# Kernel optimization log

Hardware: AMD Instinct MI355X
Metric: run time of the kernel (lower is better)

Reference implementation:

```python
import jax, jax.numpy as jnp
import numpy as np

DIM = 512
HEADS = 16
HIDDEN = 2048
EPS = 1e-5


def _layernorm(x, g, b):
    mu = jnp.mean(x, axis=-1, keepdims=True)
    var = jnp.mean((x - mu) ** 2, axis=-1, keepdims=True)
    return (x - mu) * jax.lax.rsqrt(var + EPS) * g + b


def _heads_merge(o):
    # Faithful to source: sum.reshape(B, N, D) applied to [B, H, N, pd]
    # WITHOUT transposing heads back (reproduces the original bug).
    B, H, N, pd = o.shape
    return o.reshape(B, N, H * pd)


def _self_attn(x, w, b, H):
    B, N, D = x.shape
    pd = D // H
    qkv = (x @ w + b).reshape(B, N, 3, H, pd).transpose(2, 0, 3, 1, 4)
    q, k, v = qkv[0], qkv[1], qkv[2]
    # NOTE: no 1/sqrt(pd) scaling in the source.
    s = jax.nn.softmax(jnp.einsum('bhnd,bhmd->bhnm', q, k), axis=-1)
    o = jnp.einsum('bhnm,bhmd->bhnd', s, v)  # == broadcast-multiply-and-sum in source
    return _heads_merge(o)


def _cross_attn(x1, x2, qw, qb, kvw, kvb, H):
    B, N, D = x1.shape
    pd = D // H
    q = (x2 @ qw + qb).reshape(B, N, H, pd).transpose(0, 2, 1, 3)
    kv = (x1 @ kvw + kvb).reshape(B, N, 2, H, pd).transpose(2, 0, 3, 1, 4)
    k, v = kv[0], kv[1]
    s = jax.nn.softmax(jnp.einsum('bhnd,bhmd->bhnm', q, k), axis=-1)
    o = jnp.einsum('bhnm,bhmd->bhnd', s, v)
    return _heads_merge(o)


def setup_inputs() -> dict:
    key = jax.random.key(0)
    ks = jax.random.split(key, 16)
    B, N, D, Hd = 4, 2048, DIM, HIDDEN
    s = 0.02
    return {
        'x1': jax.random.normal(ks[0], (B, N, D), jnp.float32),
        'x2': jax.random.normal(ks[1], (B, N, D), jnp.float32),
        'qkv_w': jax.random.normal(ks[2], (D, 3 * D), jnp.float32) * s,
        'qkv_b': jnp.zeros((3 * D,), jnp.float32),
        'q_w': jax.random.normal(ks[3], (D, D), jnp.float32) * s,
        'q_b': jnp.zeros((D,), jnp.float32),
        'kv_w': jax.random.normal(ks[4], (D, 2 * D), jnp.float32) * s,
        'kv_b': jnp.zeros((2 * D,), jnp.float32),
        'norm_g': jnp.ones((D,), jnp.float32),
        'norm_b': jnp.zeros((D,), jnp.float32),
        'fc1_w': jax.random.normal(ks[5], (D, Hd), jnp.float32) * s,
        'fc1_b': jnp.zeros((Hd,), jnp.float32),
        'fc2_w': jax.random.normal(ks[6], (Hd, D), jnp.float32) * s,
        'fc2_b': jnp.zeros((D,), jnp.float32),
    }


def reference(x1, x2, qkv_w, qkv_b, q_w, q_b, kv_w, kv_b, norm_g, norm_b,
              fc1_w, fc1_b, fc2_w, fc2_b):
    # CrossSelfDecoder.forward
    x = x2 + _cross_attn(x1, x2, q_w, q_b, kv_w, kv_b, HEADS)
    n = _layernorm(x, norm_g, norm_b)  # same norm params reused (as in source)
    x = n + _self_attn(n, qkv_w, qkv_b, HEADS)
    n = _layernorm(x, norm_g, norm_b)
    h = jax.nn.gelu(n @ fc1_w + fc1_b, approximate=False)
    x = n + (h @ fc2_w + fc2_b)
    return x
```

## Files before the change

### kernel.cpp

```cpp
#include <hip/hip_runtime.h>
#include <math.h>

#define DIM 512
#define HEADS 16
#define PD 32
#define NSEQ 2048
#define BATCH 4
#define HIDDEN 2048
#define LOG2E 1.44269504088896f

typedef __attribute__((ext_vector_type(8))) __bf16 bf16x8;
typedef __attribute__((ext_vector_type(4))) float f32x4;
typedef __attribute__((ext_vector_type(16))) float f32x16;

__device__ __forceinline__ ushort f2bf(float f) {
    unsigned u = __float_as_uint(f);
    u = (u + 0x7FFFu + ((u >> 16) & 1u)) >> 16;
    return (ushort)u;
}

__device__ __forceinline__ unsigned cvtpk_bf16(float lo, float hi) {
    unsigned r;
    asm("v_cvt_pk_bf16_f32 %0, %1, %2" : "=v"(r) : "v"(lo), "v"(hi));
    return r;
}

__device__ __forceinline__ float exp2_fast(float x) {
    float r;
    asm("v_exp_f32 %0, %1" : "=v"(r) : "v"(x));
    return r;
}

typedef __attribute__((address_space(1))) const unsigned int g_u32;
typedef __attribute__((address_space(3))) unsigned int l_u32;
__device__ __forceinline__ void gload16(const void* g, void* l) {
    __builtin_amdgcn_global_load_lds((g_u32*)g, (l_u32*)l, 16, 0, 0);
}

__device__ __forceinline__ float gelu_exact(float v) {
    return 0.5f * v * (1.0f + erff(v * 0.70710678118654752f));
}

__global__ __launch_bounds__(256)
void tr_all_kernel(const float* __restrict__ q_w, const float* __restrict__ kv_w,
                   const float* __restrict__ qkv_w, const float* __restrict__ fc1_w,
                   const float* __restrict__ fc2_w, ushort* __restrict__ wtb)
{
    __shared__ float t[32][33];
    const int bid = blockIdx.x;
    const float* W; ushort* Wt; int K, N, lb;
    if (bid < 256)       { W = q_w;   Wt = wtb;           K = 512;  N = 512;  lb = bid; }
    else if (bid < 768)  { W = kv_w;  Wt = wtb + 262144;  K = 512;  N = 1024; lb = bid - 256; }
    else if (bid < 1536) { W = qkv_w; Wt = wtb + 786432;  K = 512;  N = 1536; lb = bid - 768; }
    else if (bid < 2560) { W = fc1_w; Wt = wtb + 1572864; K = 512;  N = 2048; lb = bid - 1536; }
    else                 { W = fc2_w; Wt = wtb + 2621440; K = 2048; N = 512;  lb = bid - 2560; }
    const int nx = N / 32;
    const int n0 = (lb % nx) * 32, k0 = (lb / nx) * 32;
    const int tid = threadIdx.x;
    const int c = tid & 31, r0 = tid >> 5;
    #pragma unroll
    for (int i = 0; i < 4; ++i) {
        int r = r0 + i * 8;
        t[r][c] = W[(size_t)(k0 + r) * N + n0 + c];
    }
    __syncthreads();
    #pragma unroll
    for (int i = 0; i < 4; ++i) {
        int r = r0 + i * 8;
        Wt[(size_t)(n0 + r) * K + k0 + c] = f2bf(t[c][r]);
    }
}

template<int AIN, int EPI>
__global__ __launch_bounds__(256)
void mgemm(const void* __restrict__ Ap, const ushort* __restrict__ Bt,
           const float* __restrict__ bias, const float* __restrict__ resp,
           void* __restrict__ Cp, ushort* __restrict__ vtp,
           int M, int K, int Nc, int qcols, int vcol0)
{
    __shared__ __align__(16) ushort As[128 * 32];
    __shared__ __align__(16) ushort Bs[128 * 32];

    const int tid = threadIdx.x;
    const int wid = tid >> 6, ln = tid & 63;
    const int g = ln >> 4, c = ln & 15;
    const int wr = wid >> 1, wc = wid & 1;

    const int nwg = gridDim.x * gridDim.y;
    const int lid = blockIdx.y * gridDim.x + blockIdx.x;
    const int wg  = (lid & 7) * (nwg >> 3) + (lid >> 3);
    const int by = wg / gridDim.x, bx = wg % gridDim.x;
    const int row0 = by * 128, col0 = bx * 128;

    const f32x4 fzero = {0.f, 0.f, 0.f, 0.f};
    f32x4 acc[4][4];
    #pragma unroll
    for (int i = 0; i < 4; ++i)
        #pragma unroll
        for (int j = 0; j < 4; ++j) acc[i][j] = fzero;

    const int srow = tid >> 1, skh = tid & 1;
    const int w3 = (srow >> 1) & 3;
    const int ws0 = (2 * skh) ^ w3, ws1 = (2 * skh + 1) ^ w3;
    ushort* asw0 = &As[srow * 32 + ws0 * 8];
    ushort* asw1 = &As[srow * 32 + ws1 * 8];
    ushort* bsw0 = &Bs[srow * 32 + ws0 * 8];
    ushort* bsw1 = &Bs[srow * 32 + ws1 * 8];

    const int ps = (c >> 1) & 3;

    for (int k0 = 0; k0 < K; k0 += 32) {
        if (AIN == 0) {
            const float4* ap = (const float4*)((const float*)Ap
                                + (size_t)(row0 + srow) * K + k0 + skh * 16);
            float4 f0 = ap[0], f1 = ap[1], f2 = ap[2], f3 = ap[3];
            union { ushort u[16]; uint4 v[2]; } t;
            t.u[0] = f2bf(f0.x);  t.u[1] = f2bf(f0.y);  t.u[2] = f2bf(f0.z);  t.u[3] = f2bf(f0.w);
            t.u[4] = f2bf(f1.x);  t.u[5] = f2bf(f1.y);  t.u[6] = f2bf(f1.z);  t.u[7] = f2bf(f1.w);
            t.u[8] = f2bf(f2.x);  t.u[9] = f2bf(f2.y);  t.u[10] = f2bf(f2.z); t.u[11] = f2bf(f2.w);
            t.u[12] = f2bf(f3.x); t.u[13] = f2bf(f3.y); t.u[14] = f2bf(f3.z); t.u[15] = f2bf(f3.w);
            *(uint4*)asw0 = t.v[0];
            *(uint4*)asw1 = t.v[1];
        } else {
            const uint4* ap = (const uint4*)((const ushort*)Ap
                                + (size_t)(row0 + srow) * K + k0 + skh * 16);
            *(uint4*)asw0 = ap[0];
            *(uint4*)asw1 = ap[1];
        }
        {
            const uint4* bp = (const uint4*)(Bt + (size_t)(col0 + srow) * K + k0 + skh * 16);
            *(uint4*)bsw0 = bp[0];
            *(uint4*)bsw1 = bp[1];
        }
        __syncthreads();

        bf16x8 a[4], b[4];
        #pragma unroll
        for (int mt = 0; mt < 4; ++mt)
            a[mt] = *(const bf16x8*)&As[(wr * 64 + mt * 16 + c) * 32 + ((g ^ ps) * 8)];
        #pragma unroll
        for (int nt = 0; nt < 4; ++nt)
            b[nt] = *(const bf16x8*)&Bs[(wc * 64 + nt * 16 + c) * 32 + ((g ^ ps) * 8)];

        #pragma unroll
        for (int mt = 0; mt < 4; ++mt)
            #pragma unroll
            for (int nt = 0; nt < 4; ++nt)
                acc[mt][nt] = __builtin_amdgcn_mfma_f32_16x16x32_bf16(a[mt], b[nt], acc[mt][nt], 0, 0, 0);
        __syncthreads();
    }

    float bs[4];
    #pragma unroll
    for (int nt = 0; nt < 4; ++nt) bs[nt] = bias[col0 + wc * 64 + nt * 16 + c];

    #pragma unroll
    for (int mt = 0; mt < 4; ++mt) {
        const int rb = row0 + wr * 64 + mt * 16 + g * 4;
        #pragma unroll
        for (int nt = 0; nt < 4; ++nt) {
            const int col = col0 + wc * 64 + nt * 16 + c;
            if (EPI == 3 && col >= vcol0) {
                int cc = col - vcol0;
                int hh = cc >> 5, pd = cc & 31;
                int bq = rb >> 11, ntok = rb & 2047;
                union { ushort u[4]; uint2 v; } pk;
                #pragma unroll
                for (int reg = 0; reg < 4; ++reg)
                    pk.u[reg] = f2bf(acc[mt][nt][reg] + bs[nt]);
                *(uint2*)&vtp[((size_t)(bq * 16 + hh) * 32 + pd) * 2048 + ntok] = pk.v;
            } else {
                #pragma unroll
                for (int reg = 0; reg < 4; ++reg) {
                    int r = rb + reg;
                    float v = acc[mt][nt][reg] + bs[nt];
                    if (EPI == 1) {
                        ((ushort*)Cp)[(size_t)r * Nc + col] = f2bf(gelu_exact(v));
                    } else if (EPI == 2) {
                        ((float*)Cp)[(size_t)r * Nc + col] = v + resp[(size_t)r * Nc + col];
                    } else {
                        float v2 = (col < qcols) ? v * LOG2E : v;
                        ((ushort*)Cp)[(size_t)r * Nc + col] = f2bf(v2);
                    }
                }
            }
        }
    }
}

__global__ __launch_bounds__(256)
void attn_mfma_kernel(const ushort* __restrict__ qb_, int qstride, int qoff,
                      const ushort* __restrict__ kb_, int kstride, int koff,
                      const ushort* __restrict__ vtg,
                      const float* res, const float* __restrict__ gptr,
                      const float* __restrict__ bptr,
                      float* nf32, ushort* __restrict__ nb16)
{
    __shared__ __align__(16) ushort Klds[2][128 * 32];
    __shared__ __align__(16) ushort Vtlds[2][32 * 128];

    const int tid = threadIdx.x;
    const int w   = tid >> 6;
    const int ln  = tid & 63;
    const int c32 = ln & 31;
    const int hi  = ln >> 5;

    const int bid = blockIdx.x;
    const int xcd = bid & 7, jj = bid >> 3;
    const int bh = xcd + 8 * (jj >> 4);
    const int qt = jj & 15;
    const int b = bh >> 4, h = bh & 15;
    const size_t rowbase = (size_t)b * NSEQ;
    const int qt0 = qt * 128 + w * 32;
    const int n = qt0 + c32;

    bf16x8 qfrag[2];
    #pragma unroll
    for (int ph = 0; ph < 2; ++ph)
        qfrag[ph] = *(const bf16x8*)(qb_ + (rowbase + n) * qstride + qoff
                                     + h * PD + ph * 16 + hi * 8);

    const ushort* ks[2];
    const ushort* vs[2];
    int kd[2], vd[2];
    #pragma unroll
    for (int i = 0; i < 2; ++i) {
        int ch = 2 * w + i;
        int kvc = ch * 16 + (ln >> 2);
        int q4  = (ln & 3) ^ ((kvc >> 1) & 3);
        ks[i] = kb_ + (rowbase + kvc) * kstride + koff + h * PD + q4 * 8;
        kd[i] = ch * 512;
        int pdc = ch * 4 + (ln >> 4);
        int kv0 = ((ln & 15) ^ (pdc & 15)) * 8;
        vs[i] = vtg + ((size_t)bh * PD + pdc) * 2048 + kv0;
        vd[i] = ch * 512;
    }

#define STAGE(bi, trow)                                              \
    {                                                                \
        gload16(ks[0] + (size_t)(trow) * kstride, &Klds[bi][kd[0]]); \
        gload16(ks[1] + (size_t)(trow) * kstride, &Klds[bi][kd[1]]); \
        gload16(vs[0] + (trow), &Vtlds[bi][vd[0]]);                  \
        gload16(vs[1] + (trow), &Vtlds[bi][vd[1]]);                  \
    }

    f32x16 oacc, zero16;
    #pragma unroll
    for (int i = 0; i < 16; ++i) { oacc[i] = 0.f; zero16[i] = 0.f; }
    float l = 0.f;

    STAGE(0, 0);

    for (int t = 0; t < NSEQ / 128; ++t) {
        __syncthreads();
        if (t < NSEQ / 128 - 1) STAGE((t + 1) & 1, (t + 1) * 128);
        const ushort* Kb = Klds[t & 1];
        const ushort* Vb = Vtlds[t & 1];

        #pragma unroll
        for (int hh = 0; hh < 2; ++hh) {
            bf16x8 kf[2][2];
            #pragma unroll
            for (int kt = 0; kt < 2; ++kt)
                #pragma unroll
                for (int ph = 0; ph < 2; ++ph) {
                    int slot = (2 * ph + hi) ^ ((c32 >> 1) & 3);
                    kf[kt][ph] = *(const bf16x8*)&Kb[(hh * 64 + kt * 32 + c32) * 32 + slot * 8];
                }
            bf16x8 vf[4];
            #pragma unroll
            for (int j = 0; j < 4; ++j) {
                int slot = (hh * 8 + 2 * j + hi) ^ (c32 & 15);
                vf[j] = *(const bf16x8*)&Vb[c32 * 128 + slot * 8];
            }

            f32x16 st[2];
            __builtin_amdgcn_s_setprio(1);
            #pragma unroll
            for (int kt = 0; kt < 2; ++kt) {
                st[kt] = __builtin_amdgcn_mfma_f32_32x32x16_bf16(kf[kt][0], qfrag[0], zero16, 0, 0, 0);
                st[kt] = __builtin_amdgcn_mfma_f32_32x32x16_bf16(kf[kt][1], qfrag[1], st[kt], 0, 0, 0);
            }
            __builtin_amdgcn_s_setprio(0);

            float r0 = 0.f, r1 = 0.f, r2 = 0.f, r3 = 0.f;
            #pragma unroll
            for (int kt = 0; kt < 2; ++kt) {
                #pragma unroll
                for (int i = 0; i < 4; ++i) {
                    float p0 = exp2_fast(st[kt][i * 4 + 0]);
                    float p1 = exp2_fast(st[kt][i * 4 + 1]);
                    float p2 = exp2_fast(st[kt][i * 4 + 2]);
                    float p3 = exp2_fast(st[kt][i * 4 + 3]);
                    st[kt][i * 4 + 0] = p0; r0 += p0;
                    st[kt][i * 4 + 1] = p1; r1 += p1;
                    st[kt][i * 4 + 2] = p2; r2 += p2;
                    st[kt][i * 4 + 3] = p3; r3 += p3;
                }
            }
            float rsum = (r0 + r1) + (r2 + r3);
            rsum += __shfl_xor(rsum, 32);
            l += rsum;

            unsigned wpk[2][4][2];
            #pragma unroll
            for (int kt = 0; kt < 2; ++kt)
                #pragma unroll
                for (int rg = 0; rg < 4; ++rg) {
                    wpk[kt][rg][0] = cvtpk_bf16(st[kt][rg * 4 + 0], st[kt][rg * 4 + 1]);
                    wpk[kt][rg][1] = cvtpk_bf16(st[kt][rg * 4 + 2], st[kt][rg * 4 + 3]);
                }

            __builtin_amdgcn_s_setprio(1);
            #pragma unroll
            for (int j = 0; j < 4; ++j) {
                int kt = j >> 1, rg0 = 2 * (j & 1);
                unsigned x0 = wpk[kt][rg0][0], y0 = wpk[kt][rg0 + 1][0];
                unsigned x1 = wpk[kt][rg0][1], y1 = wpk[kt][rg0 + 1][1];
                asm("v_permlane32_swap_b32 %0, %1" : "+v"(x0), "+v"(y0));
                asm("v_permlane32_swap_b32 %0, %1" : "+v"(x1), "+v"(y1));
                union { unsigned u[4]; bf16x8 v; } pf;
                pf.u[0] = x0; pf.u[1] = x1; pf.u[2] = y0; pf.u[3] = y1;
                oacc = __builtin_amdgcn_mfma_f32_32x32x16_bf16(vf[j], pf.v, oacc, 0, 0, 0);
            }
            __builtin_amdgcn_s_setprio(0);
        }
    }
#undef STAGE

    const float inv = 1.0f / l;
    const int row2 = h * 128 + (n >> 4);
    const int colb = (n & 15) * PD;
    const size_t rowoff = (rowbase + row2) * DIM;

    float xv[16];
    float s = 0.f, ss = 0.f;
    #pragma unroll
    for (int ch = 0; ch < 4; ++ch) {
        float4 r4 = *(const float4*)&res[rowoff + colb + ch * 8 + hi * 4];
        #pragma unroll
        for (int q = 0; q < 4; ++q) {
            float rv = (q == 0) ? r4.x : (q == 1) ? r4.y : (q == 2) ? r4.z : r4.w;
            float x = rv + oacc[ch * 4 + q] * inv;
            xv[ch * 4 + q] = x; s += x; ss += x * x;
        }
    }
    s += __shfl_xor(s, 1);  ss += __shfl_xor(ss, 1);
    s += __shfl_xor(s, 2);  ss += __shfl_xor(ss, 2);
    s += __shfl_xor(s, 4);  ss += __shfl_xor(ss, 4);
    s += __shfl_xor(s, 8);  ss += __shfl_xor(ss, 8);
    s += __shfl_xor(s, 32); ss += __shfl_xor(ss, 32);
    float mu = s * (1.0f / DIM);
    float var = ss * (1.0f / DIM) - mu * mu;
    float rr = rsqrtf(var + 1e-5f);

    #pragma unroll
    for (int ch = 0; ch < 4; ++ch) {
        const int off = colb + ch * 8 + hi * 4;
        float4 g4 = *(const float4*)&gptr[off];
        float4 b4 = *(const float4*)&bptr[off];
        float y0 = (xv[ch * 4 + 0] - mu) * rr * g4.x + b4.x;
        float y1 = (xv[ch * 4 + 1] - mu) * rr * g4.y + b4.y;
        float y2 = (xv[ch * 4 + 2] - mu) * rr * g4.z + b4.z;
        float y3 = (xv[ch * 4 + 3] - mu) * rr * g4.w + b4.w;
        float4 yv = {y0, y1, y2, y3};
        *(float4*)&nf32[rowoff + off] = yv;
        uint2 pk = {cvtpk_bf16(y0, y1), cvtpk_bf16(y2, y3)};
        *(uint2*)&nb16[rowoff + off] = pk;
    }
}

extern "C" void kernel_launch(void* const* d_in, const int* in_sizes, int n_in,
                              void* d_out, int out_size, void* d_ws, size_t ws_size,
                              hipStream_t stream)
{
    const float* x1     = (const float*)d_in[0];
    const float* x2     = (const float*)d_in[1];
    const float* qkv_w  = (const float*)d_in[2];
    const float* qkv_b  = (const float*)d_in[3];
    const float* q_w    = (const float*)d_in[4];
    const float* q_b    = (const float*)d_in[5];
    const float* kv_w   = (const float*)d_in[6];
    const float* kv_b   = (const float*)d_in[7];
    const float* norm_g = (const float*)d_in[8];
    const float* norm_b = (const float*)d_in[9];
    const float* fc1_w  = (const float*)d_in[10];
    const float* fc1_b  = (const float*)d_in[11];
    const float* fc2_w  = (const float*)d_in[12];
    const float* fc2_b  = (const float*)d_in[13];
    float* out = (float*)d_out;
    float* ws  = (float*)d_ws;

    const int M = BATCH * NSEQ;
    const int BIG = 1 << 30;

    ushort* wtb    = (ushort*)ws;
    ushort* q_wt   = wtb;
    ushort* kv_wt  = wtb + 262144;
    ushort* qkv_wt = wtb + 786432;
    ushort* fc1_wt = wtb + 1572864;
    ushort* fc2_wt = wtb + 2621440;
    ushort* proj_u = (ushort*)(ws + (size_t)2 * 1024 * 1024);
    ushort* kvb16  = proj_u;
    ushort* qb16   = proj_u + (size_t)8192 * 1024;
    ushort* qkvb16 = proj_u;
    ushort* hbuf   = proj_u;
    ushort* VtG    = (ushort*)(ws + (size_t)21 * 512 * 1024);
    float*  n1f32  = ws + (size_t)13 * 1024 * 1024;
    ushort* n1b16  = (ushort*)(ws + (size_t)17 * 1024 * 1024);
    ushort* n2b16  = (ushort*)(ws + (size_t)19 * 1024 * 1024);

    dim3 blk(256);

    tr_all_kernel<<<dim3(3584), blk, 0, stream>>>(q_w, kv_w, qkv_w, fc1_w, fc2_w, wtb);

    mgemm<0, 3><<<dim3(1024 / 128, M / 128), blk, 0, stream>>>(
        x1, kv_wt, kv_b, nullptr, kvb16, VtG, M, DIM, 1024, 0, 512);
    mgemm<0, 3><<<dim3(512 / 128, M / 128), blk, 0, stream>>>(
        x2, q_wt, q_b, nullptr, qb16, nullptr, M, DIM, 512, 512, BIG);
    attn_mfma_kernel<<<dim3(1024), blk, 0, stream>>>(
        qb16, 512, 0, kvb16, 1024, 0, VtG, x2, norm_g, norm_b, n1f32, n1b16);

    mgemm<1, 3><<<dim3(1536 / 128, M / 128), blk, 0, stream>>>(
        n1b16, qkv_wt, qkv_b, nullptr, qkvb16, VtG, M, DIM, 1536, 512, 1024);
    attn_mfma_kernel<<<dim3(1024), blk, 0, stream>>>(
        qkvb16, 1536, 0, qkvb16, 1536, 512, VtG, n1f32, norm_g, norm_b, n1f32, n2b16);

    mgemm<1, 1><<<dim3(HIDDEN / 128, M / 128), blk, 0, stream>>>(
        n2b16, fc1_wt, fc1_b, nullptr, hbuf, nullptr, M, DIM, HIDDEN, 0, BIG);
    mgemm<1, 2><<<dim3(512 / 128, M / 128), blk, 0, stream>>>(
        hbuf, fc2_wt, fc2_b, n1f32, out, nullptr, M, HIDDEN, DIM, 0, BIG);
}
```

Measured before the change: 305.7 us.

## Double-buffer bf16 GEMMs with direct global-to-LDS loads

```diff
diff --git a/kernel.cpp b/kernel.cpp
--- a/kernel.cpp
+++ b/kernel.cpp
@@ -71,85 +71,13 @@
     }
 }
 
-template<int AIN, int EPI>
-__global__ __launch_bounds__(256)
-void mgemm(const void* __restrict__ Ap, const ushort* __restrict__ Bt,
-           const float* __restrict__ bias, const float* __restrict__ resp,
-           void* __restrict__ Cp, ushort* __restrict__ vtp,
-           int M, int K, int Nc, int qcols, int vcol0)
+template<int EPI>
+__device__ __forceinline__
+void gemm_epilogue(f32x4 (&acc)[4][4], const float* __restrict__ bias,
+                   const float* __restrict__ resp, void* __restrict__ Cp,
+                   ushort* __restrict__ vtp, int Nc, int qcols, int vcol0,
+                   int row0, int col0, int wr, int wc, int g, int c)
 {
-    __shared__ __align__(16) ushort As[128 * 32];
-    __shared__ __align__(16) ushort Bs[128 * 32];
-
-    const int tid = threadIdx.x;
-    const int wid = tid >> 6, ln = tid & 63;
-    const int g = ln >> 4, c = ln & 15;
-    const int wr = wid >> 1, wc = wid & 1;
-
-    const int nwg = gridDim.x * gridDim.y;
-    const int lid = blockIdx.y * gridDim.x + blockIdx.x;
-    const int wg  = (lid & 7) * (nwg >> 3) + (lid >> 3);
-    const int by = wg / gridDim.x, bx = wg % gridDim.x;
-    const int row0 = by * 128, col0 = bx * 128;
-
-    const f32x4 fzero = {0.f, 0.f, 0.f, 0.f};
-    f32x4 acc[4][4];
-    #pragma unroll
-    for (int i = 0; i < 4; ++i)
-        #pragma unroll
-        for (int j = 0; j < 4; ++j) acc[i][j] = fzero;
-
-    const int srow = tid >> 1, skh = tid & 1;
-    const int w3 = (srow >> 1) & 3;
-    const int ws0 = (2 * skh) ^ w3, ws1 = (2 * skh + 1) ^ w3;
-    ushort* asw0 = &As[srow * 32 + ws0 * 8];
-    ushort* asw1 = &As[srow * 32 + ws1 * 8];
-    ushort* bsw0 = &Bs[srow * 32 + ws0 * 8];
-    ushort* bsw1 = &Bs[srow * 32 + ws1 * 8];
-
-    const int ps = (c >> 1) & 3;
-
-    for (int k0 = 0; k0 < K; k0 += 32) {
-        if (AIN == 0) {
-            const float4* ap = (const float4*)((const float*)Ap
-                                + (size_t)(row0 + srow) * K + k0 + skh * 16);
-            float4 f0 = ap[0], f1 = ap[1], f2 = ap[2], f3 = ap[3];
-            union { ushort u[16]; uint4 v[2]; } t;
-            t.u[0] = f2bf(f0.x);  t.u[1] = f2bf(f0.y);  t.u[2] = f2bf(f0.z);  t.u[3] = f2bf(f0.w);
-            t.u[4] = f2bf(f1.x);  t.u[5] = f2bf(f1.y);  t.u[6] = f2bf(f1.z);  t.u[7] = f2bf(f1.w);
-            t.u[8] = f2bf(f2.x);  t.u[9] = f2bf(f2.y);  t.u[10] = f2bf(f2.z); t.u[11] = f2bf(f2.w);
-            t.u[12] = f2bf(f3.x); t.u[13] = f2bf(f3.y); t.u[14] = f2bf(f3.z); t.u[15] = f2bf(f3.w);
-            *(uint4*)asw0 = t.v[0];
-            *(uint4*)asw1 = t.v[1];
-        } else {
-            const uint4* ap = (const uint4*)((const ushort*)Ap
-                                + (size_t)(row0 + srow) * K + k0 + skh * 16);
-            *(uint4*)asw0 = ap[0];
-            *(uint4*)asw1 = ap[1];
-        }
-        {
-            const uint4* bp = (const uint4*)(Bt + (size_t)(col0 + srow) * K + k0 + skh * 16);
-            *(uint4*)bsw0 = bp[0];
-            *(uint4*)bsw1 = bp[1];
-        }
-        __syncthreads();
-
-        bf16x8 a[4], b[4];
-        #pragma unroll
-        for (int mt = 0; mt < 4; ++mt)
-            a[mt] = *(const bf16x8*)&As[(wr * 64 + mt * 16 + c) * 32 + ((g ^ ps) * 8)];
-        #pragma unroll
-        for (int nt = 0; nt < 4; ++nt)
-            b[nt] = *(const bf16x8*)&Bs[(wc * 64 + nt * 16 + c) * 32 + ((g ^ ps) * 8)];
-
-        #pragma unroll
-        for (int mt = 0; mt < 4; ++mt)
-            #pragma unroll
-            for (int nt = 0; nt < 4; ++nt)
-                acc[mt][nt] = __builtin_amdgcn_mfma_f32_16x16x32_bf16(a[mt], b[nt], acc[mt][nt], 0, 0, 0);
-        __syncthreads();
-    }
-
     float bs[4];
     #pragma unroll
     for (int nt = 0; nt < 4; ++nt) bs[nt] = bias[col0 + wc * 64 + nt * 16 + c];
@@ -188,6 +116,163 @@
     }
 }
 
+template<int EPI>
+__global__ __launch_bounds__(256)
+void mgemm(const float* __restrict__ Ap, const ushort* __restrict__ Bt,
+           const float* __restrict__ bias, const float* __restrict__ resp,
+           void* __restrict__ Cp, ushort* __restrict__ vtp,
+           int M, int K, int Nc, int qcols, int vcol0)
+{
+    __shared__ __align__(16) ushort As[128 * 32];
+    __shared__ __align__(16) ushort Bs[128 * 32];
+
+    const int tid = threadIdx.x;
+    const int wid = tid >> 6, ln = tid & 63;
+    const int g = ln >> 4, c = ln & 15;
+    const int wr = wid >> 1, wc = wid & 1;
+
+    const int nwg = gridDim.x * gridDim.y;
+    const int lid = blockIdx.y * gridDim.x + blockIdx.x;
+    const int wg  = (lid & 7) * (nwg >> 3) + (lid >> 3);
+    const int by = wg / gridDim.x, bx = wg % gridDim.x;
+    const int row0 = by * 128, col0 = bx * 128;
+
+    const f32x4 fzero = {0.f, 0.f, 0.f, 0.f};
+    f32x4 acc[4][4];
+    #pragma unroll
+    for (int i = 0; i < 4; ++i)
+        #pragma unroll
+        for (int j = 0; j < 4; ++j) acc[i][j] = fzero;
+
+    const int srow = tid >> 1, skh = tid & 1;
+    const int w3 = (srow >> 1) & 3;
+    const int ws0 = (2 * skh) ^ w3, ws1 = (2 * skh + 1) ^ w3;
+    ushort* asw0 = &As[srow * 32 + ws0 * 8];
+    ushort* asw1 = &As[srow * 32 + ws1 * 8];
+    ushort* bsw0 = &Bs[srow * 32 + ws0 * 8];
+    ushort* bsw1 = &Bs[srow * 32 + ws1 * 8];
+
+    const int ps = (c >> 1) & 3;
+
+    for (int k0 = 0; k0 < K; k0 += 32) {
+        {
+            const float4* ap = (const float4*)(Ap + (size_t)(row0 + srow) * K + k0 + skh * 16);
+            float4 f0 = ap[0], f1 = ap[1], f2 = ap[2], f3 = ap[3];
+            union { ushort u[16]; uint4 v[2]; } t;
+            t.u[0] = f2bf(f0.x);  t.u[1] = f2bf(f0.y);  t.u[2] = f2bf(f0.z);  t.u[3] = f2bf(f0.w);
+            t.u[4] = f2bf(f1.x);  t.u[5] = f2bf(f1.y);  t.u[6] = f2bf(f1.z);  t.u[7] = f2bf(f1.w);
+            t.u[8] = f2bf(f2.x);  t.u[9] = f2bf(f2.y);  t.u[10] = f2bf(f2.z); t.u[11] = f2bf(f2.w);
+            t.u[12] = f2bf(f3.x); t.u[13] = f2bf(f3.y); t.u[14] = f2bf(f3.z); t.u[15] = f2bf(f3.w);
+            *(uint4*)asw0 = t.v[0];
+            *(uint4*)asw1 = t.v[1];
+        }
+        {
+            const uint4* bp = (const uint4*)(Bt + (size_t)(col0 + srow) * K + k0 + skh * 16);
+            *(uint4*)bsw0 = bp[0];
+            *(uint4*)bsw1 = bp[1];
+        }
+        __syncthreads();
+
+        bf16x8 a[4], b[4];
+        #pragma unroll
+        for (int mt = 0; mt < 4; ++mt)
+            a[mt] = *(const bf16x8*)&As[(wr * 64 + mt * 16 + c) * 32 + ((g ^ ps) * 8)];
+        #pragma unroll
+        for (int nt = 0; nt < 4; ++nt)
+            b[nt] = *(const bf16x8*)&Bs[(wc * 64 + nt * 16 + c) * 32 + ((g ^ ps) * 8)];
+
+        #pragma unroll
+        for (int mt = 0; mt < 4; ++mt)
+            #pragma unroll
+            for (int nt = 0; nt < 4; ++nt)
+                acc[mt][nt] = __builtin_amdgcn_mfma_f32_16x16x32_bf16(a[mt], b[nt], acc[mt][nt], 0, 0, 0);
+        __syncthreads();
+    }
+
+    gemm_epilogue<EPI>(acc, bias, resp, Cp, vtp, Nc, qcols, vcol0,
+                       row0, col0, wr, wc, g, c);
+}
+
+template<int EPI>
+__global__ __launch_bounds__(256)
+void mgemm_bf(const ushort* __restrict__ Ap, const ushort* __restrict__ Bt,
+              const float* __restrict__ bias, const float* __restrict__ resp,
+              void* __restrict__ Cp, ushort* __restrict__ vtp,
+              int M, int K, int Nc, int qcols, int vcol0)
+{
+    __shared__ __align__(16) ushort As[2][128 * 32];
+    __shared__ __align__(16) ushort Bs[2][128 * 32];
+
+    const int tid = threadIdx.x;
+    const int wid = tid >> 6, ln = tid & 63;
+    const int g = ln >> 4, c = ln & 15;
+    const int wr = wid >> 1, wc = wid & 1;
+
+    const int nwg = gridDim.x * gridDim.y;
+    const int lid = blockIdx.y * gridDim.x + blockIdx.x;
+    const int wg  = (lid & 7) * (nwg >> 3) + (lid >> 3);
+    const int by = wg / gridDim.x, bx = wg % gridDim.x;
+    const int row0 = by * 128, col0 = bx * 128;
+
+    const f32x4 fzero = {0.f, 0.f, 0.f, 0.f};
+    f32x4 acc[4][4];
+    #pragma unroll
+    for (int i = 0; i < 4; ++i)
+        #pragma unroll
+        for (int j = 0; j < 4; ++j) acc[i][j] = fzero;
+
+    const ushort* asrc[2];
+    const ushort* bsrc[2];
+    int ldst[2];
+    #pragma unroll
+    for (int i = 0; i < 2; ++i) {
+        int p = i * 256 + wid * 64 + ln;
+        int row = p >> 2;
+        int q4 = (p & 3) ^ ((row >> 1) & 3);
+        asrc[i] = Ap + (size_t)(row0 + row) * K + q4 * 8;
+        bsrc[i] = Bt + (size_t)(col0 + row) * K + q4 * 8;
+        ldst[i] = (i * 256 + wid * 64) * 8;
+    }
+
+#define GSTAGE(bi, kk)                                   \
+    {                                                    \
+        gload16(asrc[0] + (kk), &As[bi][ldst[0]]);       \
+        gload16(asrc[1] + (kk), &As[bi][ldst[1]]);       \
+        gload16(bsrc[0] + (kk), &Bs[bi][ldst[0]]);       \
+        gload16(bsrc[1] + (kk), &Bs[bi][ldst[1]]);       \
+    }
+
+    const int ps = (c >> 1) & 3;
+    const int nk = K / 32;
+
+    GSTAGE(0, 0);
+
+    for (int ks = 0; ks < nk; ++ks) {
+        __syncthreads();
+        if (ks + 1 < nk) GSTAGE((ks + 1) & 1, (ks + 1) * 32);
+        const ushort* Ab = As[ks & 1];
+        const ushort* Bb = Bs[ks & 1];
+
+        bf16x8 a[4], b[4];
+        #pragma unroll
+        for (int mt = 0; mt < 4; ++mt)
+            a[mt] = *(const bf16x8*)&Ab[(wr * 64 + mt * 16 + c) * 32 + ((g ^ ps) * 8)];
+        #pragma unroll
+        for (int nt = 0; nt < 4; ++nt)
+            b[nt] = *(const bf16x8*)&Bb[(wc * 64 + nt * 16 + c) * 32 + ((g ^ ps) * 8)];
+
+        #pragma unroll
+        for (int mt = 0; mt < 4; ++mt)
+            #pragma unroll
+            for (int nt = 0; nt < 4; ++nt)
+                acc[mt][nt] = __builtin_amdgcn_mfma_f32_16x16x32_bf16(a[mt], b[nt], acc[mt][nt], 0, 0, 0);
+    }
+#undef GSTAGE
+
+    gemm_epilogue<EPI>(acc, bias, resp, Cp, vtp, Nc, qcols, vcol0,
+                       row0, col0, wr, wc, g, c);
+}
+
 __global__ __launch_bounds__(256)
 void attn_mfma_kernel(const ushort* __restrict__ qb_, int qstride, int qoff,
                       const ushort* __restrict__ kb_, int kstride, int koff,
@@ -414,20 +499,20 @@
 
     tr_all_kernel<<<dim3(3584), blk, 0, stream>>>(q_w, kv_w, qkv_w, fc1_w, fc2_w, wtb);
 
-    mgemm<0, 3><<<dim3(1024 / 128, M / 128), blk, 0, stream>>>(
+    mgemm<3><<<dim3(1024 / 128, M / 128), blk, 0, stream>>>(
         x1, kv_wt, kv_b, nullptr, kvb16, VtG, M, DIM, 1024, 0, 512);
-    mgemm<0, 3><<<dim3(512 / 128, M / 128), blk, 0, stream>>>(
+    mgemm<3><<<dim3(512 / 128, M / 128), blk, 0, stream>>>(
         x2, q_wt, q_b, nullptr, qb16, nullptr, M, DIM, 512, 512, BIG);
     attn_mfma_kernel<<<dim3(1024), blk, 0, stream>>>(
         qb16, 512, 0, kvb16, 1024, 0, VtG, x2, norm_g, norm_b, n1f32, n1b16);
 
-    mgemm<1, 3><<<dim3(1536 / 128, M / 128), blk, 0, stream>>>(
+    mgemm_bf<3><<<dim3(1536 / 128, M / 128), blk, 0, stream>>>(
         n1b16, qkv_wt, qkv_b, nullptr, qkvb16, VtG, M, DIM, 1536, 512, 1024);
     attn_mfma_kernel<<<dim3(1024), blk, 0, stream>>>(
         qkvb16, 1536, 0, qkvb16, 1536, 512, VtG, n1f32, norm_g, norm_b, n1f32, n2b16);
 
-    mgemm<1, 1><<<dim3(HIDDEN / 128, M / 128), blk, 0, stream>>>(
+    mgemm_bf<1><<<dim3(HIDDEN / 128, M / 128), blk, 0, stream>>>(
         n2b16, fc1_wt, fc1_b, nullptr, hbuf, nullptr, M, DIM, HIDDEN, 0, BIG);
-    mgemm<1, 2><<<dim3(512 / 128, M / 128), blk, 0, stream>>>(
+    mgemm_bf<2><<<dim3(512 / 128, M / 128), blk, 0, stream>>>(
         hbuf, fc2_wt, fc2_b, n1f32, out, nullptr, M, HIDDEN, DIM, 0, BIG);
 }
```

After: 289.6 us. 1.06x faster.
